# Kernel tuning notes

Hardware: AMD Instinct MI355X
Metric: run time of the kernel (lower is better)

The kernel has to match this reference:

```python
import jax, jax.numpy as jnp
import numpy as np

N_SRC = 200000
N_DST = 50000
N_EDGES = 1600000
D_IN = 256
D_OUT = 16


def setup_inputs() -> dict:
    key = jax.random.key(0)
    k1, k2, k3, k4, k5 = jax.random.split(key, 5)
    x = jax.random.normal(k1, (N_SRC, D_IN), dtype=jnp.float32)
    W = jax.random.normal(k2, (D_IN, D_OUT), dtype=jnp.float32) / np.sqrt(D_IN)
    b = jnp.zeros((D_OUT,), dtype=jnp.float32)
    edge_src = jax.random.randint(k3, (N_EDGES,), 0, N_SRC, dtype=jnp.int64)
    edge_dst = jax.random.randint(k4, (N_EDGES,), 0, N_DST, dtype=jnp.int64)
    res_n_id = jax.random.randint(k5, (N_DST,), 0, N_SRC, dtype=jnp.int64)
    return {"x": x, "W": W, "b": b, "edge_src": edge_src,
            "edge_dst": edge_dst, "res_n_id": res_n_id}


def reference(x, W, b, edge_src, edge_dst, res_n_id):
    n_src = x.shape[0]
    n_dst = res_n_id.shape[0]
    # Linear transform first (small out dim keeps edge-level traffic low).
    x_lin = x @ W                                   # [n_src, d_out]
    ones = jnp.ones(edge_src.shape, dtype=x.dtype)
    deg_src = jax.ops.segment_sum(ones, edge_src, num_segments=n_src)
    deg_dst = jax.ops.segment_sum(ones, edge_dst, num_segments=n_dst)
    # GCN symmetric normalization with self-loops (sampled bipartite block).
    norm = jax.lax.rsqrt((deg_src[edge_src] + 1.0) * (deg_dst[edge_dst] + 1.0))
    msgs = norm[:, None] * x_lin[edge_src]          # [E, d_out] irregular gather
    agg = jax.ops.segment_sum(msgs, edge_dst, num_segments=n_dst)
    # Self-loop term uses the gathered target-node features x[res_n_id].
    self_term = x_lin[res_n_id] / (deg_dst + 1.0)[:, None]
    out = agg + self_term + b                       # [n_dst, d_out]
    return jax.nn.log_softmax(out, axis=1)
```

## Files before the change

### kernel.cpp

```cpp
#include <hip/hip_runtime.h>
#include <hip/hip_bf16.h>

#define D_IN   256
#define D_OUT  16

__device__ __forceinline__ void acc4(float4& a, float xs, const float4& wv) {
  a.x += xs * wv.x; a.y += xs * wv.y; a.z += xs * wv.z; a.w += xs * wv.w;
}

__global__ __launch_bounds__(256) void xlin_deg_kernel(
    const float* __restrict__ x, const float* __restrict__ W,
    float* __restrict__ xlin,
    const int* __restrict__ es, const int* __restrict__ ed,
    float* __restrict__ deg_src, float* __restrict__ deg_dst,
    int n_src, int n_edges, int stride, int nb_gemv, int nblocks) {
  if (blockIdx.x < (unsigned)nb_gemv) {
    const int kg = threadIdx.x & 15;
    const int cg = (threadIdx.x >> 4) & 3;
    const int wv = threadIdx.x >> 6;
    const int gw = blockIdx.x * 4 + wv;
    const int total_waves = nb_gemv * 4;

    float4 wf[4][4];
#pragma unroll
    for (int j = 0; j < 4; ++j)
#pragma unroll
      for (int jj = 0; jj < 4; ++jj) {
        int r = 4 * kg + 64 * j + jj;
        wf[j][jj] = *reinterpret_cast<const float4*>(W + r * D_OUT + cg * 4);
      }

    const int npairs = n_src >> 1;
    for (int p = gw; p < npairs; p += total_waves) {
      const int r0 = 2 * p, r1 = 2 * p + 1;
      float4 xv0[4], xv1[4];
#pragma unroll
      for (int j = 0; j < 4; ++j) {
        xv0[j] = *reinterpret_cast<const float4*>(x + (size_t)r0 * D_IN + (kg + 16 * j) * 4);
        xv1[j] = *reinterpret_cast<const float4*>(x + (size_t)r1 * D_IN + (kg + 16 * j) * 4);
      }
      float4 a0 = make_float4(0.f, 0.f, 0.f, 0.f);
      float4 a1 = make_float4(0.f, 0.f, 0.f, 0.f);
#pragma unroll
      for (int j = 0; j < 4; ++j) {
        acc4(a0, xv0[j].x, wf[j][0]); acc4(a1, xv1[j].x, wf[j][0]);
        acc4(a0, xv0[j].y, wf[j][1]); acc4(a1, xv1[j].y, wf[j][1]);
        acc4(a0, xv0[j].z, wf[j][2]); acc4(a1, xv1[j].z, wf[j][2]);
        acc4(a0, xv0[j].w, wf[j][3]); acc4(a1, xv1[j].w, wf[j][3]);
      }
#pragma unroll
      for (int off = 1; off < 16; off <<= 1) {
        a0.x += __shfl_xor(a0.x, off, 16); a0.y += __shfl_xor(a0.y, off, 16);
        a0.z += __shfl_xor(a0.z, off, 16); a0.w += __shfl_xor(a0.w, off, 16);
        a1.x += __shfl_xor(a1.x, off, 16); a1.y += __shfl_xor(a1.y, off, 16);
        a1.z += __shfl_xor(a1.z, off, 16); a1.w += __shfl_xor(a1.w, off, 16);
      }
      if (kg == 0) {
        *reinterpret_cast<float4*>(xlin + (size_t)r0 * D_OUT + cg * 4) = a0;
        *reinterpret_cast<float4*>(xlin + (size_t)r1 * D_OUT + cg * 4) = a1;
      }
    }
  } else {
    const int nb_h = nblocks - nb_gemv;
    const int t0 = (blockIdx.x - nb_gemv) * 256 + threadIdx.x;
    for (int e = t0; e < n_edges; e += nb_h * 256) {
      int s = es[(size_t)e * stride];
      int d = ed[(size_t)e * stride];
      atomicAdd(&deg_src[s], 1.0f);
      atomicAdd(&deg_dst[d], 1.0f);
    }
  }
}

__global__ __launch_bounds__(256) void edge_kernel(
    const int* __restrict__ es, const int* __restrict__ ed,
    const float* __restrict__ xlin, const float* __restrict__ deg_src,
    float* __restrict__ m, int n_edges, int stride) {
  int t = blockIdx.x * 256 + threadIdx.x;
  int e = t >> 4;
  int c = t & 15;
  if (e >= n_edges) return;
  int s = es[(size_t)e * stride];
  int d = ed[(size_t)e * stride];
  float v = rsqrtf(deg_src[s] + 1.0f) * xlin[(size_t)s * D_OUT + c];
  atomicAdd(&m[(size_t)d * D_OUT + c], v);
}

__global__ __launch_bounds__(256) void finalize_kernel(
    const float* __restrict__ xlin, const int* __restrict__ rn,
    const float* __restrict__ deg_dst, const float* __restrict__ b,
    float* __restrict__ out, int n_dst, int stride) {
  int t = blockIdx.x * 256 + threadIdx.x;
  int row = t >> 4;
  int c = t & 15;
  if (row >= n_dst) return;
  int r = rn[(size_t)row * stride];
  float dd = deg_dst[row];
  float v = out[(size_t)row * D_OUT + c] * rsqrtf(dd + 1.0f)
          + xlin[(size_t)r * D_OUT + c] / (dd + 1.0f)
          + b[c];
  float mx = v;
#pragma unroll
  for (int off = 1; off < 16; off <<= 1) mx = fmaxf(mx, __shfl_xor(mx, off, 16));
  float ex = expf(v - mx);
  float sum = ex;
#pragma unroll
  for (int off = 1; off < 16; off <<= 1) sum += __shfl_xor(sum, off, 16);
  out[(size_t)row * D_OUT + c] = v - mx - logf(sum);
}

extern "C" void kernel_launch(void* const* d_in, const int* in_sizes, int n_in,
                              void* d_out, int out_size, void* d_ws, size_t ws_size,
                              hipStream_t stream) {
  const float* x  = (const float*)d_in[0];
  const float* W  = (const float*)d_in[1];
  const float* b  = (const float*)d_in[2];
  const int*   es = (const int*)d_in[3];
  const int*   ed = (const int*)d_in[4];
  const int*   rn = (const int*)d_in[5];
  float* out = (float*)d_out;

  const int n_src = in_sizes[0] / D_IN;
  const int n_dst = out_size / D_OUT;

  int stride_e = 1, n_e = in_sizes[3];
  if (in_sizes[3] == 3200000) { stride_e = 2; n_e = 1600000; }
  int stride_r = 1;
  if (in_sizes[5] == 2 * n_dst) { stride_r = 2; }

  float* xlin    = (float*)d_ws;
  float* deg_src = xlin + (size_t)n_src * D_OUT;
  float* deg_dst = deg_src + n_src;

  (void)hipMemsetAsync(deg_src, 0, (size_t)(n_src + n_dst) * sizeof(float), stream);
  (void)hipMemsetAsync(d_out, 0, (size_t)out_size * sizeof(float), stream);

  {
    const int nb_gemv = 768, nblocks = 2048;
    xlin_deg_kernel<<<nblocks, 256, 0, stream>>>(x, W, xlin, es, ed,
                                                 deg_src, deg_dst,
                                                 n_src, n_e, stride_e,
                                                 nb_gemv, nblocks);
  }
  {
    long long threads = (long long)n_e * D_OUT;
    int grid = (int)((threads + 255) / 256);
    edge_kernel<<<grid, 256, 0, stream>>>(es, ed, xlin, deg_src, out, n_e, stride_e);
  }
  {
    int threads = n_dst * D_OUT;
    int grid = (threads + 255) / 256;
    finalize_kernel<<<grid, 256, 0, stream>>>(xlin, rn, deg_dst, b, out, n_dst, stride_r);
  }
}
```

Baseline: 530.5 us.

## Fuse all stages into one cooperative persistent kernel with grid syncs

Replaces the two memsets and three kernel launches with a single cooperative kernel that zeroes buffers, runs the GEMV plus degree counting, the edge scatter and the finalize, separated by grid-wide syncs. Every block now does both GEMV rows and degree atomics instead of dedicating blocks to each role. This targets launch and memset overhead, at the cost of grid-sync barriers and a persistent grid capped at 1024 blocks. If the cooperative launch fails, it falls back to the separate-kernel path.

After: 828.5 us. 1.56x slower.

```diff
diff --git a/kernel.cpp b/kernel.cpp
--- a/kernel.cpp
+++ b/kernel.cpp
@@ -1,74 +1,139 @@
 #include <hip/hip_runtime.h>
 #include <hip/hip_bf16.h>
+#include <hip/hip_cooperative_groups.h>
+
+namespace cg = cooperative_groups;
 
 #define D_IN   256
 #define D_OUT  16
+#define NTHR   256
 
 __device__ __forceinline__ void acc4(float4& a, float xs, const float4& wv) {
   a.x += xs * wv.x; a.y += xs * wv.y; a.z += xs * wv.z; a.w += xs * wv.w;
 }
 
-__global__ __launch_bounds__(256) void xlin_deg_kernel(
+__device__ __forceinline__ void gemv_phase(
+    const float* __restrict__ x, const float* __restrict__ W,
+    float* __restrict__ xlin, int n_src, int gw, int total_waves) {
+  const int kg = threadIdx.x & 15;
+  const int cg_ = (threadIdx.x >> 4) & 3;
+
+  float4 wf[4][4];
+#pragma unroll
+  for (int j = 0; j < 4; ++j)
+#pragma unroll
+    for (int jj = 0; jj < 4; ++jj) {
+      int r = 4 * kg + 64 * j + jj;
+      wf[j][jj] = *reinterpret_cast<const float4*>(W + r * D_OUT + cg_ * 4);
+    }
+
+  const int npairs = n_src >> 1;
+  for (int p = gw; p < npairs; p += total_waves) {
+    const int r0 = 2 * p, r1 = 2 * p + 1;
+    float4 xv0[4], xv1[4];
+#pragma unroll
+    for (int j = 0; j < 4; ++j) {
+      xv0[j] = *reinterpret_cast<const float4*>(x + (size_t)r0 * D_IN + (kg + 16 * j) * 4);
+      xv1[j] = *reinterpret_cast<const float4*>(x + (size_t)r1 * D_IN + (kg + 16 * j) * 4);
+    }
+    float4 a0 = make_float4(0.f, 0.f, 0.f, 0.f);
+    float4 a1 = make_float4(0.f, 0.f, 0.f, 0.f);
+#pragma unroll
+    for (int j = 0; j < 4; ++j) {
+      acc4(a0, xv0[j].x, wf[j][0]); acc4(a1, xv1[j].x, wf[j][0]);
+      acc4(a0, xv0[j].y, wf[j][1]); acc4(a1, xv1[j].y, wf[j][1]);
+      acc4(a0, xv0[j].z, wf[j][2]); acc4(a1, xv1[j].z, wf[j][2]);
+      acc4(a0, xv0[j].w, wf[j][3]); acc4(a1, xv1[j].w, wf[j][3]);
+    }
+#pragma unroll
+    for (int off = 1; off < 16; off <<= 1) {
+      a0.x += __shfl_xor(a0.x, off, 16); a0.y += __shfl_xor(a0.y, off, 16);
+      a0.z += __shfl_xor(a0.z, off, 16); a0.w += __shfl_xor(a0.w, off, 16);
+      a1.x += __shfl_xor(a1.x, off, 16); a1.y += __shfl_xor(a1.y, off, 16);
+      a1.z += __shfl_xor(a1.z, off, 16); a1.w += __shfl_xor(a1.w, off, 16);
+    }
+    if (kg == 0) {
+      *reinterpret_cast<float4*>(xlin + (size_t)r0 * D_OUT + cg_ * 4) = a0;
+      *reinterpret_cast<float4*>(xlin + (size_t)r1 * D_OUT + cg_ * 4) = a1;
+    }
+  }
+}
+
+__device__ __forceinline__ void finalize_row(
+    const float* __restrict__ xlin, const int* __restrict__ rn,
+    const float* __restrict__ deg_dst, const float* __restrict__ b,
+    float* __restrict__ out, int row, int c, int stride_r) {
+  int r = rn[(size_t)row * stride_r];
+  float dd = deg_dst[row];
+  float v = out[(size_t)row * D_OUT + c] * rsqrtf(dd + 1.0f)
+          + xlin[(size_t)r * D_OUT + c] / (dd + 1.0f)
+          + b[c];
+  float mx = v;
+#pragma unroll
+  for (int off = 1; off < 16; off <<= 1) mx = fmaxf(mx, __shfl_xor(mx, off, 16));
+  float ex = expf(v - mx);
+  float sum = ex;
+#pragma unroll
+  for (int off = 1; off < 16; off <<= 1) sum += __shfl_xor(sum, off, 16);
+  out[(size_t)row * D_OUT + c] = v - mx - logf(sum);
+}
+
+__global__ __launch_bounds__(256) void fused_kernel(
+    const float* __restrict__ x, const float* __restrict__ W,
+    const float* __restrict__ b,
+    const int* __restrict__ es, const int* __restrict__ ed,
+    const int* __restrict__ rn,
+    float* __restrict__ out, float* __restrict__ xlin,
+    float* __restrict__ deg_src, float* __restrict__ deg_dst,
+    int n_src, int n_dst, int n_edges, int stride_e, int stride_r) {
+  cg::grid_group grid = cg::this_grid();
+  const int nblocks = gridDim.x;
+  const int tid = blockIdx.x * NTHR + threadIdx.x;
+  const int nthreads = nblocks * NTHR;
+
+  for (int i = tid; i < n_src; i += nthreads) deg_src[i] = 0.f;
+  for (int i = tid; i < n_dst; i += nthreads) deg_dst[i] = 0.f;
+  for (int i = tid; i < n_dst * D_OUT; i += nthreads) out[i] = 0.f;
+  grid.sync();
+
+  gemv_phase(x, W, xlin, n_src, blockIdx.x * 4 + (threadIdx.x >> 6), nblocks * 4);
+  for (int e = tid; e < n_edges; e += nthreads) {
+    int s = es[(size_t)e * stride_e];
+    int d = ed[(size_t)e * stride_e];
+    atomicAdd(&deg_src[s], 1.0f);
+    atomicAdd(&deg_dst[d], 1.0f);
+  }
+  grid.sync();
+
+  {
+    const int total = n_edges * D_OUT;
+    for (int t = tid; t < total; t += nthreads) {
+      int e = t >> 4;
+      int c = t & 15;
+      int s = es[(size_t)e * stride_e];
+      int d = ed[(size_t)e * stride_e];
+      float v = rsqrtf(deg_src[s] + 1.0f) * xlin[(size_t)s * D_OUT + c];
+      atomicAdd(&out[(size_t)d * D_OUT + c], v);
+    }
+  }
+  grid.sync();
+
+  for (int t = tid; t < n_dst * D_OUT; t += nthreads)
+    finalize_row(xlin, rn, deg_dst, b, out, t >> 4, t & 15, stride_r);
+}
+
+__global__ __launch_bounds__(256) void xlin_deg3_kernel(
     const float* __restrict__ x, const float* __restrict__ W,
     float* __restrict__ xlin,
     const int* __restrict__ es, const int* __restrict__ ed,
     float* __restrict__ deg_src, float* __restrict__ deg_dst,
-    int n_src, int n_edges, int stride, int nb_gemv, int nblocks) {
-  if (blockIdx.x < (unsigned)nb_gemv) {
-    const int kg = threadIdx.x & 15;
-    const int cg = (threadIdx.x >> 4) & 3;
-    const int wv = threadIdx.x >> 6;
-    const int gw = blockIdx.x * 4 + wv;
-    const int total_waves = nb_gemv * 4;
-
-    float4 wf[4][4];
-#pragma unroll
-    for (int j = 0; j < 4; ++j)
-#pragma unroll
-      for (int jj = 0; jj < 4; ++jj) {
-        int r = 4 * kg + 64 * j + jj;
-        wf[j][jj] = *reinterpret_cast<const float4*>(W + r * D_OUT + cg * 4);
-      }
-
-    const int npairs = n_src >> 1;
-    for (int p = gw; p < npairs; p += total_waves) {
-      const int r0 = 2 * p, r1 = 2 * p + 1;
-      float4 xv0[4], xv1[4];
-#pragma unroll
-      for (int j = 0; j < 4; ++j) {
-        xv0[j] = *reinterpret_cast<const float4*>(x + (size_t)r0 * D_IN + (kg + 16 * j) * 4);
-        xv1[j] = *reinterpret_cast<const float4*>(x + (size_t)r1 * D_IN + (kg + 16 * j) * 4);
-      }
-      float4 a0 = make_float4(0.f, 0.f, 0.f, 0.f);
-      float4 a1 = make_float4(0.f, 0.f, 0.f, 0.f);
-#pragma unroll
-      for (int j = 0; j < 4; ++j) {
-        acc4(a0, xv0[j].x, wf[j][0]); acc4(a1, xv1[j].x, wf[j][0]);
-        acc4(a0, xv0[j].y, wf[j][1]); acc4(a1, xv1[j].y, wf[j][1]);
-        acc4(a0, xv0[j].z, wf[j][2]); acc4(a1, xv1[j].z, wf[j][2]);
-        acc4(a0, xv0[j].w, wf[j][3]); acc4(a1, xv1[j].w, wf[j][3]);
-      }
-#pragma unroll
-      for (int off = 1; off < 16; off <<= 1) {
-        a0.x += __shfl_xor(a0.x, off, 16); a0.y += __shfl_xor(a0.y, off, 16);
-        a0.z += __shfl_xor(a0.z, off, 16); a0.w += __shfl_xor(a0.w, off, 16);
-        a1.x += __shfl_xor(a1.x, off, 16); a1.y += __shfl_xor(a1.y, off, 16);
-        a1.z += __shfl_xor(a1.z, off, 16); a1.w += __shfl_xor(a1.w, off, 16);
-      }
-      if (kg == 0) {
-        *reinterpret_cast<float4*>(xlin + (size_t)r0 * D_OUT + cg * 4) = a0;
-        *reinterpret_cast<float4*>(xlin + (size_t)r1 * D_OUT + cg * 4) = a1;
-      }
-    }
-  } else {
-    const int nb_h = nblocks - nb_gemv;
-    const int t0 = (blockIdx.x - nb_gemv) * 256 + threadIdx.x;
-    for (int e = t0; e < n_edges; e += nb_h * 256) {
-      int s = es[(size_t)e * stride];
-      int d = ed[(size_t)e * stride];
-      atomicAdd(&deg_src[s], 1.0f);
-      atomicAdd(&deg_dst[d], 1.0f);
-    }
+    int n_src, int n_edges, int stride, int nblocks) {
+  gemv_phase(x, W, xlin, n_src, blockIdx.x * 4 + (threadIdx.x >> 6), nblocks * 4);
+  for (int e = blockIdx.x * NTHR + threadIdx.x; e < n_edges; e += nblocks * NTHR) {
+    int s = es[(size_t)e * stride];
+    int d = ed[(size_t)e * stride];
+    atomicAdd(&deg_src[s], 1.0f);
+    atomicAdd(&deg_dst[d], 1.0f);
   }
 }
 
@@ -76,7 +141,7 @@
     const int* __restrict__ es, const int* __restrict__ ed,
     const float* __restrict__ xlin, const float* __restrict__ deg_src,
     float* __restrict__ m, int n_edges, int stride) {
-  int t = blockIdx.x * 256 + threadIdx.x;
+  int t = blockIdx.x * NTHR + threadIdx.x;
   int e = t >> 4;
   int c = t & 15;
   if (e >= n_edges) return;
@@ -90,23 +155,9 @@
     const float* __restrict__ xlin, const int* __restrict__ rn,
     const float* __restrict__ deg_dst, const float* __restrict__ b,
     float* __restrict__ out, int n_dst, int stride) {
-  int t = blockIdx.x * 256 + threadIdx.x;
-  int row = t >> 4;
-  int c = t & 15;
-  if (row >= n_dst) return;
-  int r = rn[(size_t)row * stride];
-  float dd = deg_dst[row];
-  float v = out[(size_t)row * D_OUT + c] * rsqrtf(dd + 1.0f)
-          + xlin[(size_t)r * D_OUT + c] / (dd + 1.0f)
-          + b[c];
-  float mx = v;
-#pragma unroll
-  for (int off = 1; off < 16; off <<= 1) mx = fmaxf(mx, __shfl_xor(mx, off, 16));
-  float ex = expf(v - mx);
-  float sum = ex;
-#pragma unroll
-  for (int off = 1; off < 16; off <<= 1) sum += __shfl_xor(sum, off, 16);
-  out[(size_t)row * D_OUT + c] = v - mx - logf(sum);
+  int t = blockIdx.x * NTHR + threadIdx.x;
+  if (t >= n_dst * D_OUT) return;
+  finalize_row(xlin, rn, deg_dst, b, out, t >> 4, t & 15, stride);
 }
 
 extern "C" void kernel_launch(void* const* d_in, const int* in_sizes, int n_in,
@@ -120,8 +171,8 @@
   const int*   rn = (const int*)d_in[5];
   float* out = (float*)d_out;
 
-  const int n_src = in_sizes[0] / D_IN;
-  const int n_dst = out_size / D_OUT;
+  int n_src = in_sizes[0] / D_IN;
+  int n_dst = out_size / D_OUT;
 
   int stride_e = 1, n_e = in_sizes[3];
   if (in_sizes[3] == 3200000) { stride_e = 2; n_e = 1600000; }
@@ -132,24 +183,48 @@
   float* deg_src = xlin + (size_t)n_src * D_OUT;
   float* deg_dst = deg_src + n_src;
 
-  (void)hipMemsetAsync(deg_src, 0, (size_t)(n_src + n_dst) * sizeof(float), stream);
-  (void)hipMemsetAsync(d_out, 0, (size_t)out_size * sizeof(float), stream);
-
+  int nblk = 0;
   {
-    const int nb_gemv = 768, nblocks = 2048;
-    xlin_deg_kernel<<<nblocks, 256, 0, stream>>>(x, W, xlin, es, ed,
-                                                 deg_src, deg_dst,
-                                                 n_src, n_e, stride_e,
-                                                 nb_gemv, nblocks);
-  }
-  {
-    long long threads = (long long)n_e * D_OUT;
-    int grid = (int)((threads + 255) / 256);
-    edge_kernel<<<grid, 256, 0, stream>>>(es, ed, xlin, deg_src, out, n_e, stride_e);
-  }
-  {
-    int threads = n_dst * D_OUT;
-    int grid = (threads + 255) / 256;
-    finalize_kernel<<<grid, 256, 0, stream>>>(xlin, rn, deg_dst, b, out, n_dst, stride_r);
-  }
-}
+    int perCU = 0;
+    hipError_t rc = hipOccupancyMaxActiveBlocksPerMultiprocessor(
+        &perCU, (const void*)fused_kernel, NTHR, 0);
+    if (rc == hipSuccess && perCU > 0) {
+      int numCU = 256;
+      (void)hipDeviceGetAttribute(&numCU, hipDeviceAttributeMultiprocessorCount, 0);
+      long long cap = (long long)perCU * numCU;
+      nblk = (int)(cap < 1024 ? cap : 1024);
+    }
+  }
+
+  hipError_t coop_rc = hipErrorUnknown;
+  if (nblk > 0) {
+    void* args[] = {
+      (void*)&x, (void*)&W, (void*)&b, (void*)&es, (void*)&ed, (void*)&rn,
+      (void*)&out, (void*)&xlin, (void*)&deg_src, (void*)&deg_dst,
+      (void*)&n_src, (void*)&n_dst, (void*)&n_e, (void*)&stride_e, (void*)&stride_r
+    };
+    coop_rc = hipLaunchCooperativeKernel((const void*)fused_kernel,
+                                         dim3(nblk), dim3(NTHR), args, 0, stream);
+  }
+
+  if (coop_rc != hipSuccess) {
+    (void)hipMemsetAsync(deg_src, 0, (size_t)(n_src + n_dst) * sizeof(float), stream);
+    (void)hipMemsetAsync(d_out, 0, (size_t)out_size * sizeof(float), stream);
+    {
+      const int grid = 1024;
+      xlin_deg3_kernel<<<grid, NTHR, 0, stream>>>(x, W, xlin, es, ed,
+                                                  deg_src, deg_dst,
+                                                  n_src, n_e, stride_e, grid);
+    }
+    {
+      long long threads = (long long)n_e * D_OUT;
+      int grid = (int)((threads + NTHR - 1) / NTHR);
+      edge_kernel<<<grid, NTHR, 0, stream>>>(es, ed, xlin, deg_src, out, n_e, stride_e);
+    }
+    {
+      int threads = n_dst * D_OUT;
+      int grid = (threads + NTHR - 1) / NTHR;
+      finalize_kernel<<<grid, NTHR, 0, stream>>>(xlin, rn, deg_dst, b, out, n_dst, stride_r);
+    }
+  }
+}
```
